# Optimization experiments

Measured on AMD Instinct MI355X. Metric: run time of the kernel, lower is better.

The kernel has to match this reference:

```python
import jax, jax.numpy as jnp
import numpy as np

COLOR_SIZE = 4
SIZE = 128
LENGTH = SIZE * SIZE * 3  # 49152


def setup_inputs() -> dict:
    key = jax.random.key(0)
    k1, k2, k3, k4 = jax.random.split(key, 4)
    example = jax.random.randint(k1, (2, SIZE, SIZE, 3), 0, COLOR_SIZE, dtype=jnp.int32)
    W_in = jax.random.normal(k2, (1, 1024), dtype=jnp.float32) * 0.02
    pos_enc = jax.random.normal(k3, (LENGTH, 1024), dtype=jnp.float32)
    W_final = jax.random.normal(k4, (1024, COLOR_SIZE), dtype=jnp.float32) * 0.02
    b_final = jnp.zeros((COLOR_SIZE,), dtype=jnp.float32)
    return {"example": example, "W_in": W_in, "pos_enc": pos_enc,
            "W_final": W_final, "b_final": b_final}


def reference(example, W_in, pos_enc, W_final, b_final):
    # example: [B, 128, 128, 3] int, values in [0, color_size)
    B = example.shape[0]
    x = example.astype(jnp.float32) / COLOR_SIZE * 2.0 - 1.0
    x = x.reshape(B, LENGTH, 1)
    x = x * 2.0 - 1.0  # second scaling, as in original call()
    x = x @ W_in  # [B, L, 1] @ [1, F] -> [B, L, F]
    x = jax.nn.relu(x + pos_enc)
    # running-average via causal cumsum; factor computed in fp16 as in original
    factor = (1.0 / jnp.arange(1, LENGTH + 1, dtype=jnp.float32))
    factor = factor.astype(jnp.float16).astype(jnp.float32)[:, None]
    x = jnp.cumsum(x, axis=-2) * factor
    x = x @ W_final + b_final  # [B, L, color_size]
    x = x.reshape(B, SIZE, SIZE, 3, COLOR_SIZE)
    return x.astype(jnp.float32)
```

## Files before the change

kernel.cpp:

```cpp
#include <hip/hip_runtime.h>
#include <math.h>

#define L_TOTAL 49152
#define NBLK 768
#define ROWS_PER_BLK 64
#define NCHUNK 32

__device__ __forceinline__ float4 f4add(float4 a, float4 b) {
  return make_float4(a.x + b.x, a.y + b.y, a.z + b.z, a.w + b.w);
}

__device__ __forceinline__ float fp16_roundtrip_pos(float x) {
  unsigned u = __float_as_uint(x);
  int e = (int)((u >> 23) & 0xffu) - 127;
  unsigned m = (u & 0x7fffffu) | 0x800000u;
  int shift = (e >= -14) ? 13 : (13 + (-14 - e));
  if (shift >= 25) return 0.0f;
  unsigned keep = m >> shift;
  unsigned rem = m & ((1u << shift) - 1u);
  unsigned halfbit = 1u << (shift - 1);
  if (rem > halfbit || (rem == halfbit && (keep & 1u))) keep++;
  return ldexpf((float)keep, e + shift - 23);
}

__global__ __launch_bounds__(256, 3) void gpart_kernel(
    const int* __restrict__ ex, const float4* __restrict__ win4,
    const float4* __restrict__ pos4, const float4* __restrict__ wf4,
    float4* __restrict__ gbuf, float4* __restrict__ pp) {
  __shared__ float4 tile[2][ROWS_PER_BLK][9];
  __shared__ float4 wtot[2][4];

  const int tid = threadIdx.x;
  const int lane = tid & 63;
  const int wv = tid >> 6;
  const int rowBase = blockIdx.x * ROWS_PER_BLK;

  const int r_st = tid >> 2;
  const int q_st = tid & 3;

  const int seg = lane >> 4;
  const int r16 = lane & 15;
  const int myrow = wv * 16 + r16;
  const int grow = rowBase + myrow;

  const float s0 = (float)ex[grow] - 3.0f;
  const float s1 = (float)ex[L_TOTAL + grow] - 3.0f;

  float4 a0 = make_float4(0.f, 0.f, 0.f, 0.f);
  float4 a1 = make_float4(0.f, 0.f, 0.f, 0.f);

  const size_t prow = (size_t)(rowBase + r_st) * 256;

  tile[0][r_st][q_st]     = pos4[prow + q_st];
  tile[0][r_st][q_st + 4] = pos4[prow + q_st + 4];
  float4 stA = pos4[prow + 8 + q_st];
  float4 stB = pos4[prow + 8 + q_st + 4];
  __syncthreads();

  for (int c = 0; c < NCHUNK; ++c) {
    if (c + 1 < NCHUNK) {
      tile[(c + 1) & 1][r_st][q_st]     = stA;
      tile[(c + 1) & 1][r_st][q_st + 4] = stB;
    }
    if (c + 2 < NCHUNK) {
      const int f4n = (c + 2) * 8;
      stA = pos4[prow + f4n + q_st];
      stB = pos4[prow + f4n + q_st + 4];
    }
    const int f4b = c * 8 + seg * 2;
    const float4 p0 = tile[c & 1][myrow][seg * 2];
    const float4 p1 = tile[c & 1][myrow][seg * 2 + 1];
    const float4 w0 = win4[f4b];
    const float4 w1 = win4[f4b + 1];
    const float pe[8] = {p0.x, p0.y, p0.z, p0.w, p1.x, p1.y, p1.z, p1.w};
    const float we[8] = {w0.x, w0.y, w0.z, w0.w, w1.x, w1.y, w1.z, w1.w};
#pragma unroll
    for (int e = 0; e < 8; ++e) {
      const float4 wf = wf4[f4b * 4 + e];
      const float t0 = fmaxf(fmaf(s0, we[e], pe[e]), 0.0f);
      const float t1 = fmaxf(fmaf(s1, we[e], pe[e]), 0.0f);
      a0.x = fmaf(t0, wf.x, a0.x); a0.y = fmaf(t0, wf.y, a0.y);
      a0.z = fmaf(t0, wf.z, a0.z); a0.w = fmaf(t0, wf.w, a0.w);
      a1.x = fmaf(t1, wf.x, a1.x); a1.y = fmaf(t1, wf.y, a1.y);
      a1.z = fmaf(t1, wf.z, a1.z); a1.w = fmaf(t1, wf.w, a1.w);
    }
    __syncthreads();
  }

#define REDUCE8(MASK)                                                   \
  a0.x += __shfl_xor(a0.x, MASK); a0.y += __shfl_xor(a0.y, MASK);       \
  a0.z += __shfl_xor(a0.z, MASK); a0.w += __shfl_xor(a0.w, MASK);       \
  a1.x += __shfl_xor(a1.x, MASK); a1.y += __shfl_xor(a1.y, MASK);       \
  a1.z += __shfl_xor(a1.z, MASK); a1.w += __shfl_xor(a1.w, MASK);
  REDUCE8(16)
  REDUCE8(32)
#undef REDUCE8

#pragma unroll
  for (int d = 1; d < 16; d <<= 1) {
    const float u0 = __shfl_up(a0.x, d), u1 = __shfl_up(a0.y, d);
    const float u2 = __shfl_up(a0.z, d), u3 = __shfl_up(a0.w, d);
    const float u4 = __shfl_up(a1.x, d), u5 = __shfl_up(a1.y, d);
    const float u6 = __shfl_up(a1.z, d), u7 = __shfl_up(a1.w, d);
    if (r16 >= d) {
      a0.x += u0; a0.y += u1; a0.z += u2; a0.w += u3;
      a1.x += u4; a1.y += u5; a1.z += u6; a1.w += u7;
    }
  }

  float4 t0, t1;
  t0.x = __shfl(a0.x, 15); t0.y = __shfl(a0.y, 15);
  t0.z = __shfl(a0.z, 15); t0.w = __shfl(a0.w, 15);
  t1.x = __shfl(a1.x, 15); t1.y = __shfl(a1.y, 15);
  t1.z = __shfl(a1.z, 15); t1.w = __shfl(a1.w, 15);
  if (lane == 0) { wtot[0][wv] = t0; wtot[1][wv] = t1; }
  __syncthreads();
  float4 o0 = make_float4(0.f, 0.f, 0.f, 0.f);
  float4 o1 = make_float4(0.f, 0.f, 0.f, 0.f);
  for (int j = 0; j < wv; ++j) {
    o0 = f4add(o0, wtot[0][j]);
    o1 = f4add(o1, wtot[1][j]);
  }
  a0 = f4add(a0, o0);
  a1 = f4add(a1, o1);

  if (seg == 0) {
    gbuf[grow] = a0;
    gbuf[L_TOTAL + grow] = a1;
  }
  if (tid == 255) {
    pp[blockIdx.x] = a0;
    pp[NBLK + blockIdx.x] = a1;
  }
}

__global__ __launch_bounds__(128, 8) void finish_kernel(
    const float4* __restrict__ gbuf, const float4* __restrict__ pp,
    const float* __restrict__ bfin, float4* __restrict__ out4) {
  const int tid = threadIdx.x;
  const int bb = tid >> 6;
  const int i = tid & 63;
  const int bid = blockIdx.x;

  float4 q = make_float4(0.f, 0.f, 0.f, 0.f);
  for (int j = i; j < bid; j += 64) q = f4add(q, pp[bb * NBLK + j]);
#pragma unroll
  for (int off = 32; off > 0; off >>= 1) {
    q.x += __shfl_xor(q.x, off); q.y += __shfl_xor(q.y, off);
    q.z += __shfl_xor(q.z, off); q.w += __shfl_xor(q.w, off);
  }

  const int row = bid * ROWS_PER_BLK + i;
  const float4 v = f4add(gbuf[(size_t)bb * L_TOTAL + row], q);
  const float factor = fp16_roundtrip_pos(1.0f / (float)(row + 1));
  float4 o;
  o.x = fmaf(v.x, factor, bfin[0]);
  o.y = fmaf(v.y, factor, bfin[1]);
  o.z = fmaf(v.z, factor, bfin[2]);
  o.w = fmaf(v.w, factor, bfin[3]);
  out4[(size_t)bb * L_TOTAL + row] = o;
}

extern "C" void kernel_launch(void* const* d_in, const int* in_sizes, int n_in,
                              void* d_out, int out_size, void* d_ws, size_t ws_size,
                              hipStream_t stream) {
  const int* ex = (const int*)d_in[0];
  const float4* win4 = (const float4*)d_in[1];
  const float4* pos4 = (const float4*)d_in[2];
  const float4* wf4 = (const float4*)d_in[3];
  const float* bfin = (const float*)d_in[4];
  float4* out4 = (float4*)d_out;

  float4* gbuf = (float4*)d_ws;
  float4* pp = gbuf + (size_t)2 * L_TOTAL;

  gpart_kernel<<<NBLK, 256, 0, stream>>>(ex, win4, pos4, wf4, gbuf, pp);
  finish_kernel<<<NBLK, 128, 0, stream>>>(gbuf, pp, bfin, out4);
}
```

Measured before the change: 48.04 us.

## Fuse two-pass scan into single kernel with decoupled inter-block prefix flags

Merges the partial-sum kernel and the finish kernel into one launch. Each block publishes its block total with a release flag, and its first wavefront spins on all predecessor flags to build the exclusive prefix before writing the final scaled output. This removes the second kernel launch and the round trip of the per-row intermediate buffer through global memory. In exchange it adds a memset launch, relies on forward progress of earlier blocks, and late blocks may spin-wait.

```diff
diff --git a/kernel.cpp b/kernel.cpp
--- a/kernel.cpp
+++ b/kernel.cpp
@@ -23,17 +23,20 @@
   return ldexpf((float)keep, e + shift - 23);
 }
 
-__global__ __launch_bounds__(256, 3) void gpart_kernel(
+__global__ __launch_bounds__(256, 3) void fused_kernel(
     const int* __restrict__ ex, const float4* __restrict__ win4,
     const float4* __restrict__ pos4, const float4* __restrict__ wf4,
-    float4* __restrict__ gbuf, float4* __restrict__ pp) {
+    const float* __restrict__ bfin, float4* __restrict__ out4,
+    float* __restrict__ aggf, int* __restrict__ flags) {
   __shared__ float4 tile[2][ROWS_PER_BLK][9];
   __shared__ float4 wtot[2][4];
+  __shared__ float4 boffs[2];
 
   const int tid = threadIdx.x;
   const int lane = tid & 63;
   const int wv = tid >> 6;
-  const int rowBase = blockIdx.x * ROWS_PER_BLK;
+  const int bid = blockIdx.x;
+  const int rowBase = bid * ROWS_PER_BLK;
 
   const int r_st = tid >> 2;
   const int q_st = tid & 3;
@@ -124,41 +127,64 @@
   a0 = f4add(a0, o0);
   a1 = f4add(a1, o1);
 
+  if (tid == 255) {
+    const float v[8] = {a0.x, a0.y, a0.z, a0.w, a1.x, a1.y, a1.z, a1.w};
+#pragma unroll
+    for (int k = 0; k < 8; ++k)
+      __hip_atomic_store(&aggf[(size_t)bid * 8 + k], v[k], __ATOMIC_RELAXED,
+                         __HIP_MEMORY_SCOPE_AGENT);
+    __hip_atomic_store(&flags[bid], 1, __ATOMIC_RELEASE,
+                       __HIP_MEMORY_SCOPE_AGENT);
+  }
+
+  if (wv == 0) {
+    float4 q0 = make_float4(0.f, 0.f, 0.f, 0.f);
+    float4 q1 = make_float4(0.f, 0.f, 0.f, 0.f);
+    for (int base = 0; base < bid; base += 64) {
+      const int j = base + lane;
+      if (j < bid) {
+        while (__hip_atomic_load(&flags[j], __ATOMIC_ACQUIRE,
+                                 __HIP_MEMORY_SCOPE_AGENT) == 0) {
+          __builtin_amdgcn_s_sleep(1);
+        }
+        const float* aj = &aggf[(size_t)j * 8];
+        q0.x += __hip_atomic_load(aj + 0, __ATOMIC_RELAXED, __HIP_MEMORY_SCOPE_AGENT);
+        q0.y += __hip_atomic_load(aj + 1, __ATOMIC_RELAXED, __HIP_MEMORY_SCOPE_AGENT);
+        q0.z += __hip_atomic_load(aj + 2, __ATOMIC_RELAXED, __HIP_MEMORY_SCOPE_AGENT);
+        q0.w += __hip_atomic_load(aj + 3, __ATOMIC_RELAXED, __HIP_MEMORY_SCOPE_AGENT);
+        q1.x += __hip_atomic_load(aj + 4, __ATOMIC_RELAXED, __HIP_MEMORY_SCOPE_AGENT);
+        q1.y += __hip_atomic_load(aj + 5, __ATOMIC_RELAXED, __HIP_MEMORY_SCOPE_AGENT);
+        q1.z += __hip_atomic_load(aj + 6, __ATOMIC_RELAXED, __HIP_MEMORY_SCOPE_AGENT);
+        q1.w += __hip_atomic_load(aj + 7, __ATOMIC_RELAXED, __HIP_MEMORY_SCOPE_AGENT);
+      }
+    }
+#pragma unroll
+    for (int off = 32; off > 0; off >>= 1) {
+      q0.x += __shfl_xor(q0.x, off); q0.y += __shfl_xor(q0.y, off);
+      q0.z += __shfl_xor(q0.z, off); q0.w += __shfl_xor(q0.w, off);
+      q1.x += __shfl_xor(q1.x, off); q1.y += __shfl_xor(q1.y, off);
+      q1.z += __shfl_xor(q1.z, off); q1.w += __shfl_xor(q1.w, off);
+    }
+    if (lane == 0) { boffs[0] = q0; boffs[1] = q1; }
+  }
+  __syncthreads();
+
   if (seg == 0) {
-    gbuf[grow] = a0;
-    gbuf[L_TOTAL + grow] = a1;
-  }
-  if (tid == 255) {
-    pp[blockIdx.x] = a0;
-    pp[NBLK + blockIdx.x] = a1;
-  }
-}
-
-__global__ __launch_bounds__(128, 8) void finish_kernel(
-    const float4* __restrict__ gbuf, const float4* __restrict__ pp,
-    const float* __restrict__ bfin, float4* __restrict__ out4) {
-  const int tid = threadIdx.x;
-  const int bb = tid >> 6;
-  const int i = tid & 63;
-  const int bid = blockIdx.x;
-
-  float4 q = make_float4(0.f, 0.f, 0.f, 0.f);
-  for (int j = i; j < bid; j += 64) q = f4add(q, pp[bb * NBLK + j]);
-#pragma unroll
-  for (int off = 32; off > 0; off >>= 1) {
-    q.x += __shfl_xor(q.x, off); q.y += __shfl_xor(q.y, off);
-    q.z += __shfl_xor(q.z, off); q.w += __shfl_xor(q.w, off);
-  }
-
-  const int row = bid * ROWS_PER_BLK + i;
-  const float4 v = f4add(gbuf[(size_t)bb * L_TOTAL + row], q);
-  const float factor = fp16_roundtrip_pos(1.0f / (float)(row + 1));
-  float4 o;
-  o.x = fmaf(v.x, factor, bfin[0]);
-  o.y = fmaf(v.y, factor, bfin[1]);
-  o.z = fmaf(v.z, factor, bfin[2]);
-  o.w = fmaf(v.w, factor, bfin[3]);
-  out4[(size_t)bb * L_TOTAL + row] = o;
+    const float4 v0 = f4add(a0, boffs[0]);
+    const float4 v1 = f4add(a1, boffs[1]);
+    const float factor = fp16_roundtrip_pos(1.0f / (float)(grow + 1));
+    float4 u0, u1;
+    u0.x = fmaf(v0.x, factor, bfin[0]);
+    u0.y = fmaf(v0.y, factor, bfin[1]);
+    u0.z = fmaf(v0.z, factor, bfin[2]);
+    u0.w = fmaf(v0.w, factor, bfin[3]);
+    u1.x = fmaf(v1.x, factor, bfin[0]);
+    u1.y = fmaf(v1.y, factor, bfin[1]);
+    u1.z = fmaf(v1.z, factor, bfin[2]);
+    u1.w = fmaf(v1.w, factor, bfin[3]);
+    out4[grow] = u0;
+    out4[L_TOTAL + grow] = u1;
+  }
 }
 
 extern "C" void kernel_launch(void* const* d_in, const int* in_sizes, int n_in,
@@ -171,9 +197,10 @@
   const float* bfin = (const float*)d_in[4];
   float4* out4 = (float4*)d_out;
 
-  float4* gbuf = (float4*)d_ws;
-  float4* pp = gbuf + (size_t)2 * L_TOTAL;
-
-  gpart_kernel<<<NBLK, 256, 0, stream>>>(ex, win4, pos4, wf4, gbuf, pp);
-  finish_kernel<<<NBLK, 128, 0, stream>>>(gbuf, pp, bfin, out4);
-}
+  float* aggf = (float*)d_ws;
+  int* flags = (int*)(aggf + (size_t)NBLK * 8);
+
+  hipMemsetAsync(flags, 0, NBLK * sizeof(int), stream);
+  fused_kernel<<<NBLK, 256, 0, stream>>>(ex, win4, pos4, wf4, bfin, out4,
+                                         aggf, flags);
+}
```

After: 106.2 us. 121% more time.
